# Performance work log

Hardware: AMD Instinct MI355X
Metric: run time of the kernel (lower is better)

The kernel has to match this reference:

```python
import jax, jax.numpy as jnp
import numpy as np

# Scaled Llama backbone (NF4 dequant-matmul == dense matmul math) + LoRA(q,v) + cls head
L, V, D, H, F, R, C = 4, 32000, 2048, 16, 8192, 16, 3
HD = D // H  # 128, matches real Llama head_dim
ALPHA_OVER_R = 32.0 / R
EPS = 1e-5
NEG = -1e9


def setup_inputs() -> dict:
    B, S = 2, 1024
    keys = iter(jax.random.split(jax.random.key(0), 40))

    def rn(shape, s=0.02):
        return jax.random.normal(next(keys), shape, dtype=jnp.float32) * s

    return {
        "input_ids": jax.random.randint(next(keys), (B, S), 0, V),
        "attention_mask": jnp.ones((B, S), dtype=jnp.int32),
        "embed": rn((V, D)),
        "Wq": rn((L, D, D)), "Wk": rn((L, D, D)), "Wv": rn((L, D, D)), "Wo": rn((L, D, D)),
        "Aq": rn((L, R, D)), "Bq": rn((L, D, R)), "Av": rn((L, R, D)), "Bv": rn((L, D, R)),
        "Wg": rn((L, F, D)), "Wu": rn((L, F, D)), "Wd": rn((L, D, F)),
        "norm1": jnp.ones((L, D)), "norm2": jnp.ones((L, D)), "final_norm": jnp.ones((D,)),
        "head_W1": rn((D, D)), "head_b1": jnp.zeros((D,)),
        "head_W2": rn((C, D)), "head_b2": jnp.zeros((C,)),
    }


def _rms(x, w):
    return x * w * jax.lax.rsqrt(jnp.mean(x * x, -1, keepdims=True) + EPS)


def _rope_tables(S):
    inv = 1.0 / (10000.0 ** (jnp.arange(0, HD, 2, dtype=jnp.float32) / HD))
    f = jnp.outer(jnp.arange(S, dtype=jnp.float32), inv)  # [S, HD//2]
    emb = jnp.concatenate([f, f], -1)                      # [S, HD]
    return jnp.cos(emb), jnp.sin(emb)


def _rot(x):
    return jnp.concatenate([-x[..., HD // 2:], x[..., :HD // 2]], -1)


def reference(input_ids, attention_mask, embed, Wq, Wk, Wv, Wo, Aq, Bq, Av, Bv,
              Wg, Wu, Wd, norm1, norm2, final_norm, head_W1, head_b1, head_W2, head_b2):
    B, S = input_ids.shape
    x = embed[input_ids]                                   # [B,S,D]
    cos, sin = _rope_tables(S)
    causal = jnp.tril(jnp.ones((S, S), dtype=bool))
    mask = jnp.where(causal[None, None], 0.0, NEG) \
        + (1.0 - attention_mask.astype(jnp.float32))[:, None, None, :] * NEG  # [B,1,S,S]

    for l in range(L):  # small fixed layer count
        h = _rms(x, norm1[l])

        def proj(W):
            return jnp.einsum('bsd,ed->bse', h, W)

        def lora(A, Bm):
            return ALPHA_OVER_R * jnp.einsum('bsr,er->bse', jnp.einsum('bsd,rd->bsr', h, A), Bm)

        q = (proj(Wq[l]) + lora(Aq[l], Bq[l])).reshape(B, S, H, HD)
        k = proj(Wk[l]).reshape(B, S, H, HD)
        v = (proj(Wv[l]) + lora(Av[l], Bv[l])).reshape(B, S, H, HD)
        q = q * cos[None, :, None, :] + _rot(q) * sin[None, :, None, :]
        k = k * cos[None, :, None, :] + _rot(k) * sin[None, :, None, :]

        scores = jnp.einsum('bqhd,bkhd->bhqk', q, k) / np.float32(np.sqrt(HD)) + mask
        attn = jax.nn.softmax(scores, -1)
        o = jnp.einsum('bhqk,bkhd->bqhd', attn, v).reshape(B, S, D)
        x = x + jnp.einsum('bsd,ed->bse', o, Wo[l])

        h2 = _rms(x, norm2[l])
        g = jnp.einsum('bsd,fd->bsf', h2, Wg[l])
        u = jnp.einsum('bsd,fd->bsf', h2, Wu[l])
        x = x + jnp.einsum('bsf,df->bsd', jax.nn.silu(g) * u, Wd[l])

    x = _rms(x, final_norm)
    # LlamaForSequenceClassification pooling at last non-pad token; score = Identity
    idx = jnp.sum(attention_mask, -1) - 1
    pooled = x[jnp.arange(B), idx].astype(jnp.float32)     # [B, D]
    # head_layer (dropout = identity in eval)
    h = jnp.tanh(pooled @ head_W1.T + head_b1)
    return h @ head_W2.T + head_b2                          # [B, C]
```

## Files before the change

### kernel.cpp

```cpp
#include <hip/hip_runtime.h>

#define NLAYER 4
#define DMODEL 2048
#define NHEAD  16
#define HEADD  128
#define FFDIM  8192
#define RLORA  16
#define SEQLEN 1024
#define NBATCH 2
#define NTOK   (NBATCH*SEQLEN)
#define QKVS   6144

typedef __bf16 bf16x8 __attribute__((ext_vector_type(8)));
typedef float  f32x4  __attribute__((ext_vector_type(4)));
typedef unsigned short us8 __attribute__((ext_vector_type(8)));

__device__ __forceinline__ unsigned short f2b(float f) {
  unsigned int u = __builtin_bit_cast(unsigned int, f);
  u += 0x7FFFu + ((u >> 16) & 1u);
  return (unsigned short)(u >> 16);
}
__device__ __forceinline__ float b2f(unsigned short s) {
  unsigned int u = ((unsigned int)s) << 16;
  return __builtin_bit_cast(float, u);
}
__device__ __forceinline__ int vswz(int d) {
  return (((d >> 2) & 7) ^ ((d & 3) << 1)) << 4;
}
typedef __attribute__((address_space(1))) const void* gas_t;
typedef __attribute__((address_space(3))) void* las_t;
__device__ __forceinline__ void gload16(const void* g, void* l) {
  __builtin_amdgcn_global_load_lds((gas_t)g, (las_t)l, 16, 0, 0);
}

__global__ void k_embed(const int* __restrict__ ids, const float* __restrict__ emb,
                        float* __restrict__ x) {
  int row = blockIdx.x;
  int id = ids[row];
  const float4* src = (const float4*)(emb + (size_t)id * DMODEL);
  float4* dst = (float4*)(x + (size_t)row * DMODEL);
  for (int i = threadIdx.x; i < DMODEL / 4; i += 256) dst[i] = src[i];
}

__global__ void k_cvt16(const float* __restrict__ s, unsigned short* __restrict__ d, int n8) {
  int stride = gridDim.x * 256;
  for (int i = blockIdx.x * 256 + threadIdx.x; i < n8; i += stride) {
    size_t si = (size_t)i * 2;
    float4 a = ((const float4*)s)[si];
    float4 b = ((const float4*)s)[si + 1];
    us8 o;
    o[0]=f2b(a.x); o[1]=f2b(a.y); o[2]=f2b(a.z); o[3]=f2b(a.w);
    o[4]=f2b(b.x); o[5]=f2b(b.y); o[6]=f2b(b.z); o[7]=f2b(b.w);
    ((us8*)d)[i] = o;
  }
}

__global__ void k_cvtqkv(const float* __restrict__ Wq, const float* __restrict__ Wk,
                         const float* __restrict__ Wv, unsigned short* __restrict__ d) {
  const size_t DD8 = (size_t)DMODEL * DMODEL / 8;
  const int n8 = (int)(NLAYER * 3 * DD8);
  int stride = gridDim.x * 256;
  for (int i = blockIdx.x * 256 + threadIdx.x; i < n8; i += stride) {
    int blk = i >> 19;
    int lay = blk / 3;
    int ten = blk - lay * 3;
    int off = i & ((1 << 19) - 1);
    const float* s = (ten == 0 ? Wq : ten == 1 ? Wk : Wv) + (size_t)lay * DMODEL * DMODEL;
    float4 a = ((const float4*)s)[(size_t)off * 2];
    float4 b = ((const float4*)s)[(size_t)off * 2 + 1];
    us8 o;
    o[0]=f2b(a.x); o[1]=f2b(a.y); o[2]=f2b(a.z); o[3]=f2b(a.w);
    o[4]=f2b(b.x); o[5]=f2b(b.y); o[6]=f2b(b.z); o[7]=f2b(b.w);
    ((us8*)(d))[(size_t)i] = o;
  }
}

__global__ void k_rmsnorm(const float* __restrict__ x, const float* __restrict__ w,
                          unsigned short* __restrict__ h) {
  int row = blockIdx.x, t = threadIdx.x;
  const float* xr = x + (size_t)row * DMODEL;
  float4 a = ((const float4*)xr)[t];
  float4 b = ((const float4*)xr)[t + 256];
  float ss = a.x*a.x + a.y*a.y + a.z*a.z + a.w*a.w
           + b.x*b.x + b.y*b.y + b.z*b.z + b.w*b.w;
  for (int m = 32; m; m >>= 1) ss += __shfl_xor(ss, m);
  __shared__ float red[4];
  if ((t & 63) == 0) red[t >> 6] = ss;
  __syncthreads();
  ss = red[0] + red[1] + red[2] + red[3];
  float rs = rsqrtf(ss * (1.0f / DMODEL) + 1e-5f);
  float4 wa = ((const float4*)w)[t];
  float4 wb = ((const float4*)w)[t + 256];
  ushort4 oa, ob;
  oa.x = f2b(a.x * wa.x * rs); oa.y = f2b(a.y * wa.y * rs);
  oa.z = f2b(a.z * wa.z * rs); oa.w = f2b(a.w * wa.w * rs);
  ob.x = f2b(b.x * wb.x * rs); ob.y = f2b(b.y * wb.y * rs);
  ob.z = f2b(b.z * wb.z * rs); ob.w = f2b(b.w * wb.w * rs);
  ushort4* hr = (ushort4*)(h + (size_t)row * DMODEL);
  hr[t] = oa;
  hr[t + 256] = ob;
}

__global__ __launch_bounds__(512, 4)
void k_ffn(const unsigned short* __restrict__ A, const unsigned short* __restrict__ Bgw,
           const unsigned short* __restrict__ Buw, unsigned short* __restrict__ act,
           int N, int K, int ldc) {
  __shared__ unsigned short As[8192];
  __shared__ unsigned short Gs[8192];
  __shared__ unsigned short Us[8192];
  const int t = threadIdx.x, l = t & 63, w = t >> 6;
  const int wm = w >> 2, wn = w & 3;
  const int nbx = gridDim.x;
  const int nmt = gridDim.y;
  const int nwg = nbx * nmt;
  const int bid = blockIdx.y * nbx + blockIdx.x;
  const int sid = (bid & 7) * (nwg >> 3) + (bid >> 3);
  const int m0 = (sid % nmt) << 7;
  const int n0 = (sid / nmt) << 7;
  const int srow = (w << 3) + (l >> 3);
  const int gcol = 8 * ((l & 7) ^ ((srow >> 1) & 7));
  const unsigned short* Ap = A   + (size_t)(m0 + srow) * K + gcol;
  const unsigned short* Gp = Bgw + (size_t)(n0 + srow) * K + gcol;
  const unsigned short* Up = Buw + (size_t)(n0 + srow) * K + gcol;
  const size_t r64K = (size_t)64 * K;
  unsigned short* AsW = As + (w << 9);
  unsigned short* GsW = Gs + (w << 9);
  unsigned short* UsW = Us + (w << 9);
  const int cl = l & 15, lh = l >> 4;
  const int fR = (cl >> 1) & 7;
  f32x4 ag[4][2], au[4][2];
  #pragma unroll
  for (int mi = 0; mi < 4; mi++)
    #pragma unroll
    for (int ni = 0; ni < 2; ni++) {
      f32x4 z = {0.f,0.f,0.f,0.f};
      ag[mi][ni] = z; au[mi][ni] = z;
    }

  for (int kt = 0; kt < K; kt += 64) {
    gload16(Ap + kt,          AsW);
    gload16(Ap + kt + r64K,   AsW + 4096);
    gload16(Gp + kt,          GsW);
    gload16(Gp + kt + r64K,   GsW + 4096);
    gload16(Up + kt,          UsW);
    gload16(Up + kt + r64K,   UsW + 4096);
    __syncthreads();
    #pragma unroll
    for (int kh = 0; kh < 2; kh++) {
      const int so = ((kh * 4 + lh) ^ fR) << 4;
      bf16x8 af[4], bg[2], bu[2];
      #pragma unroll
      for (int mi = 0; mi < 4; mi++)
        af[mi] = *(const bf16x8*)((const char*)As + (wm*64 + mi*16 + cl) * 128 + so);
      #pragma unroll
      for (int ni = 0; ni < 2; ni++) {
        bg[ni] = *(const bf16x8*)((const char*)Gs + (wn*32 + ni*16 + cl) * 128 + so);
        bu[ni] = *(const bf16x8*)((const char*)Us + (wn*32 + ni*16 + cl) * 128 + so);
      }
      #pragma unroll
      for (int mi = 0; mi < 4; mi++)
        #pragma unroll
        for (int ni = 0; ni < 2; ni++) {
          ag[mi][ni] = __builtin_amdgcn_mfma_f32_16x16x32_bf16(af[mi], bg[ni], ag[mi][ni], 0, 0, 0);
          au[mi][ni] = __builtin_amdgcn_mfma_f32_16x16x32_bf16(af[mi], bu[ni], au[mi][ni], 0, 0, 0);
        }
    }
    __syncthreads();
  }
  const int rbase = lh << 2;
  #pragma unroll
  for (int mi = 0; mi < 4; mi++) {
    #pragma unroll
    for (int ni = 0; ni < 2; ni++) {
      #pragma unroll
      for (int rr = 0; rr < 4; rr++) {
        int row = m0 + wm * 64 + mi * 16 + rbase + rr;
        int col = n0 + wn * 32 + ni * 16 + cl;
        float gv = ag[mi][ni][rr];
        float uv = au[mi][ni][rr];
        float val = gv / (1.0f + __expf(-gv)) * uv;
        act[(size_t)row * ldc + col] = f2b(val);
      }
    }
  }
}

template<int MODE>
__global__ __launch_bounds__(256, 4)
void k_gemm6(const unsigned short* __restrict__ A, const unsigned short* __restrict__ B,
             float* __restrict__ Cf, unsigned short* __restrict__ Cb,
             const float* __restrict__ Res, const unsigned short* __restrict__ Gaux,
             int N, int K, int ldc) {
  __shared__ unsigned short As[4096];
  __shared__ unsigned short Bs[8192];
  const int t = threadIdx.x, l = t & 63, w = t >> 6;
  const int nbx = gridDim.x;
  const int nmt = gridDim.y;
  const int bid = blockIdx.y * nbx + blockIdx.x;
  const int xcd = bid & 7;
  const int local = bid >> 3;
  const int cm = nmt >> 2;
  const int cn = nbx >> 1;
  const int m0 = ((xcd & 3) * cm + (local % cm)) << 6;
  const int n0 = ((xcd >> 2) * cn + (local / cm)) << 7;
  const int srow = (w << 3) + (l >> 3);
  const int gcol = 8 * ((l & 7) ^ ((srow >> 1) & 7));
  const unsigned short* Ag = A + (size_t)(m0 + srow) * K + gcol;
  const unsigned short* Bg = B + (size_t)(n0 + srow) * K + gcol;
  const size_t r32K = (size_t)32 * K;
  unsigned short* AsW = As + (w << 9);
  unsigned short* BsW = Bs + (w << 9);
  const int cl = l & 15, lh = l >> 4;
  const int fR = (cl >> 1) & 7;
  f32x4 acc[4][2];
  #pragma unroll
  for (int mi = 0; mi < 4; mi++)
    #pragma unroll
    for (int ni = 0; ni < 2; ni++) { f32x4 z = {0.f,0.f,0.f,0.f}; acc[mi][ni] = z; }

  for (int kt = 0; kt < K; kt += 64) {
    gload16(Ag + kt,          AsW);
    gload16(Ag + kt +   r32K, AsW + 2048);
    gload16(Bg + kt,          BsW);
    gload16(Bg + kt +   r32K, BsW + 2048);
    gload16(Bg + kt + 2*r32K, BsW + 4096);
    gload16(Bg + kt + 3*r32K, BsW + 6144);
    __syncthreads();
    #pragma unroll
    for (int kh = 0; kh < 2; kh++) {
      const int so = ((kh * 4 + lh) ^ fR) << 4;
      bf16x8 af[4], bf[2];
      #pragma unroll
      for (int mi = 0; mi < 4; mi++)
        af[mi] = *(const bf16x8*)((const char*)As + (mi*16 + cl) * 128 + so);
      #pragma unroll
      for (int ni = 0; ni < 2; ni++)
        bf[ni] = *(const bf16x8*)((const char*)Bs + (w*32 + ni*16 + cl) * 128 + so);
      #pragma unroll
      for (int mi = 0; mi < 4; mi++)
        #pragma unroll
        for (int ni = 0; ni < 2; ni++)
          acc[mi][ni] = __builtin_amdgcn_mfma_f32_16x16x32_bf16(af[mi], bf[ni], acc[mi][ni], 0, 0, 0);
    }
    __syncthreads();
  }
  const int rbase = lh << 2;
  #pragma unroll
  for (int mi = 0; mi < 4; mi++) {
    #pragma unroll
    for (int ni = 0; ni < 2; ni++) {
      #pragma unroll
      for (int rr = 0; rr < 4; rr++) {
        int row = m0 + mi * 16 + rbase + rr;
        int col = n0 + w * 32 + ni * 16 + cl;
        size_t idx = (size_t)row * ldc + col;
        float val = acc[mi][ni][rr];
        if constexpr (MODE == 0) Cf[idx] = val;
        if constexpr (MODE == 1) Cf[idx] = val + Res[idx];
        if constexpr (MODE == 2) Cb[idx] = f2b(val);
        if constexpr (MODE == 3) {
          float gv = b2f(Gaux[idx]);
          val *= gv / (1.0f + __expf(-gv));
          Cb[idx] = f2b(val);
        }
      }
    }
  }
}

__global__ __launch_bounds__(256, 4)
void k_gemm7(const unsigned short* __restrict__ A, const unsigned short* __restrict__ B,
             unsigned short* __restrict__ qb, unsigned short* __restrict__ kb,
             unsigned short* __restrict__ vb,
             const float* __restrict__ ct, const float* __restrict__ st,
             int K,
             const float* __restrict__ ltq, const float* __restrict__ ltv,
             const float* __restrict__ lbq, const float* __restrict__ lbv) {
  __shared__ unsigned short As[4096];
  __shared__ unsigned short Bs[8192];
  const int t = threadIdx.x, l = t & 63, w = t >> 6;
  const int nbx = gridDim.x;
  const int nmt = gridDim.y;
  const int nwg = nbx * nmt;
  const int bid = blockIdx.y * nbx + blockIdx.x;
  const int sid = (bid & 7) * (nwg >> 3) + (bid >> 3);
  const int m0 = (sid % nmt) << 6;
  const int n0 = (sid / nmt) << 7;
  const int srow = (w << 3) + (l >> 3);
  const int gcol = 8 * ((l & 7) ^ ((srow >> 1) & 7));
  const unsigned short* Ag = A + (size_t)(m0 + srow) * K + gcol;
  const unsigned short* Bg = B + (size_t)(n0 + srow) * K + gcol;
  const size_t r32K = (size_t)32 * K;
  unsigned short* AsW = As + (w << 9);
  unsigned short* BsW = Bs + (w << 9);
  const int cl = l & 15, lh = l >> 4;
  const int fR = (cl >> 1) & 7;
  f32x4 acc[4][2];
  #pragma unroll
  for (int mi = 0; mi < 4; mi++)
    #pragma unroll
    for (int ni = 0; ni < 2; ni++) { f32x4 z = {0.f,0.f,0.f,0.f}; acc[mi][ni] = z; }

  for (int kt = 0; kt < K; kt += 64) {
    gload16(Ag + kt,          AsW);
    gload16(Ag + kt +   r32K, AsW + 2048);
    gload16(Bg + kt,          BsW);
    gload16(Bg + kt +   r32K, BsW + 2048);
    gload16(Bg + kt + 2*r32K, BsW + 4096);
    gload16(Bg + kt + 3*r32K, BsW + 6144);
    __syncthreads();
    #pragma unroll
    for (int kh = 0; kh < 2; kh++) {
      const int so = ((kh * 4 + lh) ^ fR) << 4;
      bf16x8 af[4], bf[2];
      #pragma unroll
      for (int mi = 0; mi < 4; mi++)
        af[mi] = *(const bf16x8*)((const char*)As + (mi*16 + cl) * 128 + so);
      #pragma unroll
      for (int ni = 0; ni < 2; ni++)
        bf[ni] = *(const bf16x8*)((const char*)Bs + (w*16 + ni*64 + cl) * 128 + so);
      #pragma unroll
      for (int mi = 0; mi < 4; mi++)
        #pragma unroll
        for (int ni = 0; ni < 2; ni++)
          acc[mi][ni] = __builtin_amdgcn_mfma_f32_16x16x32_bf16(af[mi], bf[ni], acc[mi][ni], 0, 0, 0);
    }
    __syncthreads();
  }
  const int rbase = lh << 2;
  const int i0 = (w << 4) + cl;
  const int col_lo = n0 + i0;
  const int reg = n0 >> 11;
  const float* lt = nullptr;
  const float* lb_lo = nullptr;
  const float* lb_hi = nullptr;
  if (reg == 0)      { lt = ltq; lb_lo = lbq + (size_t)col_lo * RLORA;
                                 lb_hi = lbq + (size_t)(col_lo + 64) * RLORA; }
  else if (reg == 2) { lt = ltv; lb_lo = lbv + (size_t)(col_lo - 4096) * RLORA;
                                 lb_hi = lbv + (size_t)(col_lo - 4096 + 64) * RLORA; }
  float4 bl0={0,0,0,0}, bl1=bl0, bl2=bl0, bl3=bl0;
  float4 bh0=bl0, bh1=bl0, bh2=bl0, bh3=bl0;
  if (lt) {
    bl0 = ((const float4*)lb_lo)[0]; bl1 = ((const float4*)lb_lo)[1];
    bl2 = ((const float4*)lb_lo)[2]; bl3 = ((const float4*)lb_lo)[3];
    bh0 = ((const float4*)lb_hi)[0]; bh1 = ((const float4*)lb_hi)[1];
    bh2 = ((const float4*)lb_hi)[2]; bh3 = ((const float4*)lb_hi)[3];
  }
  unsigned short* outp = (reg == 0 ? qb : reg == 1 ? kb : vb);
  const int ocol = col_lo - reg * 2048;
  #pragma unroll
  for (int mi = 0; mi < 4; mi++) {
    #pragma unroll
    for (int rr = 0; rr < 4; rr++) {
      int row = m0 + mi * 16 + rbase + rr;
      float lo = acc[mi][0][rr];
      float hi = acc[mi][1][rr];
      if (lt) {
        const float4* tr = (const float4*)(lt + (size_t)row * RLORA);
        float4 t0 = tr[0], t1 = tr[1], t2 = tr[2], t3 = tr[3];
        lo += 2.0f * (t0.x*bl0.x + t0.y*bl0.y + t0.z*bl0.z + t0.w*bl0.w
                    + t1.x*bl1.x + t1.y*bl1.y + t1.z*bl1.z + t1.w*bl1.w
                    + t2.x*bl2.x + t2.y*bl2.y + t2.z*bl2.z + t2.w*bl2.w
                    + t3.x*bl3.x + t3.y*bl3.y + t3.z*bl3.z + t3.w*bl3.w);
        hi += 2.0f * (t0.x*bh0.x + t0.y*bh0.y + t0.z*bh0.z + t0.w*bh0.w
                    + t1.x*bh1.x + t1.y*bh1.y + t1.z*bh1.z + t1.w*bh1.w
                    + t2.x*bh2.x + t2.y*bh2.y + t2.z*bh2.z + t2.w*bh2.w
                    + t3.x*bh3.x + t3.y*bh3.y + t3.z*bh3.z + t3.w*bh3.w);
      }
      if (reg != 2) {
        int s = row & (SEQLEN - 1);
        float c = ct[s * 64 + i0], sn = st[s * 64 + i0];
        float nlo = lo * c - hi * sn;
        float nhi = hi * c + lo * sn;
        lo = nlo; hi = nhi;
      }
      outp[(size_t)row * DMODEL + ocol]      = f2b(lo);
      outp[(size_t)row * DMODEL + ocol + 64] = f2b(hi);
    }
  }
}

template<int MODE>
__global__ __launch_bounds__(256, 2)
void k_gemm(const unsigned short* __restrict__ A, const void* __restrict__ Bv,
            float* __restrict__ Cf, unsigned short* __restrict__ Cb,
            const float* __restrict__ Res, const unsigned short* __restrict__ Gaux,
            int N, int K, int ldc) {
  __shared__ unsigned char lds[128 * 32 * 2 * 2];
  unsigned char* As = lds;
  unsigned char* Bs = lds + 128 * 32 * 2;
  const int t = threadIdx.x;
  const int l = t & 63, w = t >> 6;
  const int wr = w >> 1, wc = w & 1;
  const int m0 = blockIdx.y << 7, n0 = blockIdx.x << 7;
  const int sr = t >> 1, skh = (t & 1) << 4;
  const int sByte = sr * 64 + (skh << 1);
  const int sSwz = (sr & 3) << 4;
  const unsigned short* Ap = A + (size_t)(m0 + sr) * K + skh;
  const float* Bp32 = (const float*)Bv + (size_t)(n0 + sr) * K + skh;
  const int kOff = (((l >> 4) << 4)) ^ ((l & 3) << 4);
  const int arow = wr * 64 + (l & 15);
  const int brow = wc * 64 + (l & 15);
  f32x4 acc[4][4];
  #pragma unroll
  for (int mi = 0; mi < 4; mi++)
    #pragma unroll
    for (int ni = 0; ni < 4; ni++) { f32x4 z = {0.f,0.f,0.f,0.f}; acc[mi][ni] = z; }

  for (int kt = 0; kt < K; kt += 32) {
    uint4 a0 = *(const uint4*)(Ap + kt);
    uint4 a1 = *(const uint4*)(Ap + kt + 8);
    *(uint4*)(As + ((sByte)      ^ sSwz)) = a0;
    *(uint4*)(As + ((sByte + 16) ^ sSwz)) = a1;
    float4 f0 = *(const float4*)(Bp32 + kt);
    float4 f1 = *(const float4*)(Bp32 + kt + 4);
    float4 f2 = *(const float4*)(Bp32 + kt + 8);
    float4 f3 = *(const float4*)(Bp32 + kt + 12);
    us8 q0, q1;
    q0[0]=f2b(f0.x); q0[1]=f2b(f0.y); q0[2]=f2b(f0.z); q0[3]=f2b(f0.w);
    q0[4]=f2b(f1.x); q0[5]=f2b(f1.y); q0[6]=f2b(f1.z); q0[7]=f2b(f1.w);
    q1[0]=f2b(f2.x); q1[1]=f2b(f2.y); q1[2]=f2b(f2.z); q1[3]=f2b(f2.w);
    q1[4]=f2b(f3.x); q1[5]=f2b(f3.y); q1[6]=f2b(f3.z); q1[7]=f2b(f3.w);
    *(us8*)(Bs + ((sByte)      ^ sSwz)) = q0;
    *(us8*)(Bs + ((sByte + 16) ^ sSwz)) = q1;
    __syncthreads();
    bf16x8 af[4], bfr[4];
    #pragma unroll
    for (int i = 0; i < 4; i++) {
      af[i]  = *(const bf16x8*)(As + (arow + 16 * i) * 64 + kOff);
      bfr[i] = *(const bf16x8*)(Bs + (brow + 16 * i) * 64 + kOff);
    }
    #pragma unroll
    for (int mi = 0; mi < 4; mi++)
      #pragma unroll
      for (int ni = 0; ni < 4; ni++)
        acc[mi][ni] = __builtin_amdgcn_mfma_f32_16x16x32_bf16(af[mi], bfr[ni], acc[mi][ni], 0, 0, 0);
    __syncthreads();
  }
  const int rbase = (l >> 4) << 2;
  const int cl = l & 15;
  #pragma unroll
  for (int mi = 0; mi < 4; mi++) {
    #pragma unroll
    for (int ni = 0; ni < 4; ni++) {
      #pragma unroll
      for (int rr = 0; rr < 4; rr++) {
        int row = m0 + wr * 64 + mi * 16 + rbase + rr;
        int col = n0 + wc * 64 + ni * 16 + cl;
        size_t idx = (size_t)row * ldc + col;
        float val = acc[mi][ni][rr];
        if constexpr (MODE == 0) Cf[idx] = val;
        if constexpr (MODE == 1) Cf[idx] = val + Res[idx];
        if constexpr (MODE == 2) Cb[idx] = f2b(val);
        if constexpr (MODE == 3) {
          float gv = b2f(Gaux[idx]);
          val *= gv / (1.0f + __expf(-gv));
          Cb[idx] = f2b(val);
        }
      }
    }
  }
}

__global__ void k_lora_down2(const unsigned short* __restrict__ h,
                             const float* __restrict__ Aq, const float* __restrict__ Av,
                             float* __restrict__ tbq, float* __restrict__ tbv) {
  int t = threadIdx.x;
  int m = blockIdx.x * 8 + (t >> 5), r = t & 31;
  const float* ar = (r < 16) ? (Aq + (size_t)r * DMODEL)
                             : (Av + (size_t)(r - 16) * DMODEL);
  const unsigned short* hr = h + (size_t)m * DMODEL;
  float acc = 0.f;
  for (int d = 0; d < DMODEL; d += 4) {
    ushort4 hv = *(const ushort4*)(hr + d);
    float4 av = *(const float4*)(ar + d);
    acc += b2f(hv.x)*av.x + b2f(hv.y)*av.y + b2f(hv.z)*av.z + b2f(hv.w)*av.w;
  }
  if (r < 16) tbq[(size_t)m * RLORA + r] = acc;
  else        tbv[(size_t)m * RLORA + (r - 16)] = acc;
}

__global__ void k_lora_down(const unsigned short* __restrict__ h, const float* __restrict__ Am,
                            float* __restrict__ tb) {
  int t = threadIdx.x;
  int m = blockIdx.x * 16 + (t >> 4), r = t & 15;
  const unsigned short* hr = h + (size_t)m * DMODEL;
  const float* ar = Am + (size_t)r * DMODEL;
  float acc = 0.f;
  for (int d = 0; d < DMODEL; d += 4) {
    ushort4 hv = *(const ushort4*)(hr + d);
    float4 av = *(const float4*)(ar + d);
    acc += b2f(hv.x)*av.x + b2f(hv.y)*av.y + b2f(hv.z)*av.z + b2f(hv.w)*av.w;
  }
  tb[(size_t)m * RLORA + r] = acc;
}

__global__ void k_lora_up(const float* __restrict__ tb, const float* __restrict__ Bm,
                          float* __restrict__ out, int ldc) {
  int tid = blockIdx.x * 256 + threadIdx.x;
  int m = tid >> 11, e = tid & (DMODEL - 1);
  const float* tr = tb + (size_t)m * RLORA;
  const float* br = Bm + (size_t)e * RLORA;
  float acc = 0.f;
  #pragma unroll
  for (int r = 0; r < RLORA; r += 4) {
    float4 tv = *(const float4*)(tr + r);
    float4 bv = *(const float4*)(br + r);
    acc += tv.x*bv.x + tv.y*bv.y + tv.z*bv.z + tv.w*bv.w;
  }
  out[(size_t)m * ldc + e] += 2.0f * acc;
}

__global__ void k_rope_table(float* __restrict__ ct, float* __restrict__ st) {
  int tid = blockIdx.x * 256 + threadIdx.x;
  int s = tid >> 6, i = tid & 63;
  float inv = __expf(-((float)i / 64.0f) * logf(10000.0f));
  float ang = (float)s * inv;
  ct[tid] = cosf(ang);
  st[tid] = sinf(ang);
}

__global__ void k_rope2(const float* __restrict__ qkv,
                        const float* __restrict__ ct, const float* __restrict__ st,
                        unsigned short* __restrict__ qb, unsigned short* __restrict__ kb,
                        unsigned short* __restrict__ vb) {
  int tid = blockIdx.x * 256 + threadIdx.x;
  int i = tid & 63;
  int hh = (tid >> 6) & (NHEAD - 1);
  int s = (tid >> 10) & (SEQLEN - 1);
  int b = tid >> 20;
  size_t ibase = ((size_t)(b * SEQLEN + s)) * QKVS + hh * HEADD;
  size_t obase = ((size_t)(b * SEQLEN + s)) * DMODEL + hh * HEADD;
  float c = ct[s * 64 + i], sn = st[s * 64 + i];
  float q0 = qkv[ibase + i], q1 = qkv[ibase + i + 64];
  qb[obase + i]      = f2b(q0 * c - q1 * sn);
  qb[obase + i + 64] = f2b(q1 * c + q0 * sn);
  float k0 = qkv[ibase + 2048 + i], k1 = qkv[ibase + 2048 + i + 64];
  kb[obase + i]      = f2b(k0 * c - k1 * sn);
  kb[obase + i + 64] = f2b(k1 * c + k0 * sn);
  vb[obase + i]      = f2b(qkv[ibase + 4096 + i]);
  vb[obase + i + 64] = f2b(qkv[ibase + 4096 + i + 64]);
}

__global__ __launch_bounds__(256, 2)
void k_attn_bf16(const unsigned short* __restrict__ qbp, const unsigned short* __restrict__ kbp,
                 const unsigned short* __restrict__ vbp, const int* __restrict__ am,
                 unsigned short* __restrict__ o, int vstride) {
  __shared__ unsigned char Kls[64 * 256];
  __shared__ unsigned char Vls[128 * 128];
  __shared__ unsigned char Pls[64 * 128];
  const int qt = blockIdx.x, hh = blockIdx.y, b = blockIdx.z;
  const int t = threadIdx.x, l = t & 63, w = t >> 6;
  const int cl = l & 15, lh = l >> 4;
  const int rbase = lh << 2;

  for (int ii = 0; ii < 4; ii++) {
    int idx = t + 256 * ii; int row = idx >> 4; int c = idx & 15;
    uint4 u = *(const uint4*)(qbp + ((size_t)(b*SEQLEN + qt*64 + row)) * DMODEL + hh * HEADD + c * 8);
    *(uint4*)(Kls + ((row * 256 + c * 16) ^ ((row & 7) << 4))) = u;
  }
  __syncthreads();
  bf16x8 qf[4];
  {
    int row = w * 16 + cl;
    int swz = (row & 7) << 4;
    #pragma unroll
    for (int kt = 0; kt < 4; kt++)
      qf[kt] = *(const bf16x8*)(Kls + ((row * 256 + kt * 64 + lh * 16) ^ swz));
  }

  f32x4 oacc[8];
  #pragma unroll
  for (int i = 0; i < 8; i++) { f32x4 z = {0.f,0.f,0.f,0.f}; oacc[i] = z; }
  float mrun[4], lrun[4];
  #pragma unroll
  for (int r = 0; r < 4; r++) { mrun[r] = -3e38f; lrun[r] = 0.f; }

  for (int kb = 0; kb <= qt; kb++) {
    __syncthreads();
    for (int ii = 0; ii < 4; ii++) {
      int idx = t + 256 * ii; int row = idx >> 4; int c = idx & 15;
      uint4 u = *(const uint4*)(kbp + ((size_t)(b*SEQLEN + kb*64 + row)) * DMODEL + hh * HEADD + c * 8);
      *(uint4*)(Kls + ((row * 256 + c * 16) ^ ((row & 7) << 4))) = u;
    }
    for (int ii = 0; ii < 4; ii++) {
      int idx = t + 256 * ii;
      int n = idx >> 4, dc = idx & 15;
      uint4 a = *(const uint4*)(vbp + ((size_t)(b*SEQLEN + kb*64 + n)) * vstride + hh * HEADD + dc * 8);
      uint4 p;
      p.x = __shfl_xor(a.x, 16); p.y = __shfl_xor(a.y, 16);
      p.z = __shfl_xor(a.z, 16); p.w = __shfl_xor(a.w, 16);
      if (!(l & 16)) {
        int d0 = dc * 8, nb = n * 2;
        unsigned int wd[8];
        wd[0] = (a.x & 0xffffu) | (p.x << 16);
        wd[1] = (a.x >> 16)     | (p.x & 0xffff0000u);
        wd[2] = (a.y & 0xffffu) | (p.y << 16);
        wd[3] = (a.y >> 16)     | (p.y & 0xffff0000u);
        wd[4] = (a.z & 0xffffu) | (p.z << 16);
        wd[5] = (a.z >> 16)     | (p.z & 0xffff0000u);
        wd[6] = (a.w & 0xffffu) | (p.w << 16);
        wd[7] = (a.w >> 16)     | (p.w & 0xffff0000u);
        #pragma unroll
        for (int e = 0; e < 8; e++)
          *(unsigned int*)(Vls + (((d0 + e) * 128 + nb) ^ vswz(d0 + e))) = wd[e];
      }
    }
    __syncthreads();
    f32x4 sacc[4];
    #pragma unroll
    for (int nt = 0; nt < 4; nt++) { f32x4 z = {0.f,0.f,0.f,0.f}; sacc[nt] = z; }
    #pragma unroll
    for (int kt = 0; kt < 4; kt++) {
      #pragma unroll
      for (int nt = 0; nt < 4; nt++) {
        int row = nt * 16 + cl;
        bf16x8 kf = *(const bf16x8*)(Kls + ((row * 256 + kt * 64 + lh * 16) ^ ((row & 7) << 4)));
        sacc[nt] = __builtin_amdgcn_mfma_f32_16x16x32_bf16(qf[kt], kf, sacc[nt], 0, 0, 0);
      }
    }
    float p[4][4];
    float mt[4] = {-3e38f, -3e38f, -3e38f, -3e38f};
    #pragma unroll
    for (int nt = 0; nt < 4; nt++) {
      int kg = kb * 64 + nt * 16 + cl;
      float pad = (1.0f - (float)am[b * SEQLEN + kg]) * (-1e9f);
      #pragma unroll
      for (int r = 0; r < 4; r++) {
        int qg = qt * 64 + w * 16 + rbase + r;
        float s = sacc[nt][r] * 0.08838834764831845f + pad;
        if (kg > qg) s = -1e30f;
        p[nt][r] = s;
        mt[r] = fmaxf(mt[r], s);
      }
    }
    #pragma unroll
    for (int r = 0; r < 4; r++) {
      float m = mt[r];
      m = fmaxf(m, __shfl_xor(m, 1)); m = fmaxf(m, __shfl_xor(m, 2));
      m = fmaxf(m, __shfl_xor(m, 4)); m = fmaxf(m, __shfl_xor(m, 8));
      mt[r] = m;
    }
    float corr[4];
    #pragma unroll
    for (int r = 0; r < 4; r++) {
      float mnew = fmaxf(mrun[r], mt[r]);
      corr[r] = __expf(mrun[r] - mnew);
      mrun[r] = mnew;
    }
    float ps[4] = {0.f, 0.f, 0.f, 0.f};
    #pragma unroll
    for (int nt = 0; nt < 4; nt++)
      #pragma unroll
      for (int r = 0; r < 4; r++) {
        p[nt][r] = __expf(p[nt][r] - mrun[r]);
        ps[r] += p[nt][r];
      }
    #pragma unroll
    for (int r = 0; r < 4; r++) {
      float s = ps[r];
      s += __shfl_xor(s, 1); s += __shfl_xor(s, 2);
      s += __shfl_xor(s, 4); s += __shfl_xor(s, 8);
      lrun[r] = lrun[r] * corr[r] + s;
    }
    #pragma unroll
    for (int nt = 0; nt < 4; nt++)
      #pragma unroll
      for (int r = 0; r < 4; r++) {
        int row = w * 16 + rbase + r;
        *(unsigned short*)(Pls + ((row * 128 + (nt * 16 + cl) * 2) ^ ((row & 7) << 4))) = f2b(p[nt][r]);
      }
    #pragma unroll
    for (int dt = 0; dt < 8; dt++)
      #pragma unroll
      for (int r = 0; r < 4; r++) oacc[dt][r] *= corr[r];
    {
      int prow = w * 16 + cl, pswz = (prow & 7) << 4;
      bf16x8 pf0 = *(const bf16x8*)(Pls + ((prow * 128 +  0 + lh * 16) ^ pswz));
      bf16x8 pf1 = *(const bf16x8*)(Pls + ((prow * 128 + 64 + lh * 16) ^ pswz));
      #pragma unroll
      for (int dt = 0; dt < 8; dt++) {
        int drow = dt * 16 + cl;
        bf16x8 vf0 = *(const bf16x8*)(Vls + ((drow * 128 +  0 + lh * 16) ^ vswz(drow)));
        bf16x8 vf1 = *(const bf16x8*)(Vls + ((drow * 128 + 64 + lh * 16) ^ vswz(drow)));
        oacc[dt] = __builtin_amdgcn_mfma_f32_16x16x32_bf16(pf0, vf0, oacc[dt], 0, 0, 0);
        oacc[dt] = __builtin_amdgcn_mfma_f32_16x16x32_bf16(pf1, vf1, oacc[dt], 0, 0, 0);
      }
    }
  }
  size_t obase = (((size_t)b * SEQLEN + qt * 64 + w * 16) * NHEAD + hh) * HEADD;
  #pragma unroll
  for (int r = 0; r < 4; r++) {
    float inv = 1.0f / lrun[r];
    int row = rbase + r;
    #pragma unroll
    for (int dt = 0; dt < 8; dt++)
      o[obase + (size_t)row * (NHEAD * HEADD) + dt * 16 + cl] = f2b(oacc[dt][r] * inv);
  }
}

__global__ void k_pool(const float* __restrict__ x, const int* __restrict__ am,
                       const float* __restrict__ fn, float* __restrict__ pooled) {
  int b = blockIdx.x, t = threadIdx.x;
  __shared__ float red[4];
  float fc = 0.f;
  for (int i = t; i < SEQLEN; i += 256) fc += (float)am[b * SEQLEN + i];
  for (int m = 32; m; m >>= 1) fc += __shfl_xor(fc, m);
  if ((t & 63) == 0) red[t >> 6] = fc;
  __syncthreads();
  int idx = (int)(red[0] + red[1] + red[2] + red[3]) - 1;
  const float* xr = x + ((size_t)b * SEQLEN + idx) * DMODEL;
  float4 a = ((const float4*)xr)[t], c = ((const float4*)xr)[t + 256];
  float ss = a.x*a.x + a.y*a.y + a.z*a.z + a.w*a.w
           + c.x*c.x + c.y*c.y + c.z*c.z + c.w*c.w;
  for (int m = 32; m; m >>= 1) ss += __shfl_xor(ss, m);
  __syncthreads();
  if ((t & 63) == 0) red[t >> 6] = ss;
  __syncthreads();
  ss = red[0] + red[1] + red[2] + red[3];
  float rs = rsqrtf(ss * (1.0f / DMODEL) + 1e-5f);
  float4 w0 = ((const float4*)fn)[t], w1 = ((const float4*)fn)[t + 256];
  float4 o0, o1;
  o0.x = a.x*rs*w0.x; o0.y = a.y*rs*w0.y; o0.z = a.z*rs*w0.z; o0.w = a.w*rs*w0.w;
  o1.x = c.x*rs*w1.x; o1.y = c.y*rs*w1.y; o1.z = c.z*rs*w1.z; o1.w = c.w*rs*w1.w;
  ((float4*)(pooled + (size_t)b * DMODEL))[t] = o0;
  ((float4*)(pooled + (size_t)b * DMODEL))[t + 256] = o1;
}

__global__ void k_head1(const float* __restrict__ pooled, const float* __restrict__ W1,
                        const float* __restrict__ b1, float* __restrict__ h1) {
  int bi = blockIdx.x;
  int b = bi >> 3, e = ((bi & 7) << 8) + threadIdx.x;
  const float* pr = pooled + (size_t)b * DMODEL;
  const float* wr = W1 + (size_t)e * DMODEL;
  float acc = 0.f;
  for (int d = 0; d < DMODEL; d += 4) {
    float4 pv = *(const float4*)(pr + d);
    float4 wv = *(const float4*)(wr + d);
    acc += pv.x*wv.x + pv.y*wv.y + pv.z*wv.z + pv.w*wv.w;
  }
  h1[(size_t)b * DMODEL + e] = tanhf(acc + b1[e]);
}

__global__ void k_head2(const float* __restrict__ h1, const float* __restrict__ W2,
                        const float* __restrict__ b2, float* __restrict__ out) {
  int bi = blockIdx.x;
  int b = bi / 3, c = bi % 3;
  int l = threadIdx.x;
  float acc = 0.f;
  for (int e = l; e < DMODEL; e += 64)
    acc += h1[(size_t)b * DMODEL + e] * W2[(size_t)c * DMODEL + e];
  for (int m = 32; m; m >>= 1) acc += __shfl_xor(acc, m);
  if (l == 0) out[b * 3 + c] = acc + b2[c];
}

__global__ void k_sentinel(float* out) {
  if (threadIdx.x < 6) out[threadIdx.x] = -12345.0f;
}

extern "C" void kernel_launch(void* const* d_in, const int* in_sizes, int n_in,
                              void* d_out, int out_size, void* d_ws, size_t ws_size,
                              hipStream_t stream) {
  const int*   ids = (const int*)d_in[0];
  const int*   am  = (const int*)d_in[1];
  const float* emb = (const float*)d_in[2];
  const float* Wq  = (const float*)d_in[3];
  const float* Wk  = (const float*)d_in[4];
  const float* Wv  = (const float*)d_in[5];
  const float* Wo  = (const float*)d_in[6];
  const float* Aq  = (const float*)d_in[7];
  const float* Bq  = (const float*)d_in[8];
  const float* Av  = (const float*)d_in[9];
  const float* Bv  = (const float*)d_in[10];
  const float* Wg  = (const float*)d_in[11];
  const float* Wu  = (const float*)d_in[12];
  const float* Wd  = (const float*)d_in[13];
  const float* n1  = (const float*)d_in[14];
  const float* n2  = (const float*)d_in[15];
  const float* fn  = (const float*)d_in[16];
  const float* hW1 = (const float*)d_in[17];
  const float* hb1 = (const float*)d_in[18];
  const float* hW2 = (const float*)d_in[19];
  const float* hb2 = (const float*)d_in[20];
  float* out = (float*)d_out;

  const size_t XOFF    = 0;
  const size_t HOFF    = 16777216;
  const size_t QBOFF   = 25165824;
  const size_t KBOFF   = 33554432;
  const size_t VBOFF   = 41943040;
  const size_t OOFF    = 50331648;
  const size_t GOFF    = 58720256;
  const size_t ACTOFF  = 92274688;
  const size_t QKV32OFF= 125829120;
  const size_t TOFF    = 176160768;
  const size_t NEED = TOFF + 131072 + 131072 + 262144 + 262144 + 16384 + 16384;
  if (ws_size < NEED) {
    k_sentinel<<<1, 64, 0, stream>>>(out);
    return;
  }
  const size_t W16OFF   = (NEED + 255) & ~(size_t)255;
  const size_t W16BYTES = 536870912ull;
  const bool   use16    = ws_size >= W16OFF + W16BYTES;

  char* ws = (char*)d_ws;
  float*          x     = (float*)(ws + XOFF);
  unsigned short* h     = (unsigned short*)(ws + HOFF);
  unsigned short* qb    = (unsigned short*)(ws + QBOFF);
  unsigned short* kb    = (unsigned short*)(ws + KBOFF);
  unsigned short* vb    = (unsigned short*)(ws + VBOFF);
  unsigned short* o     = (unsigned short*)(ws + OOFF);
  unsigned short* g     = (unsigned short*)(ws + GOFF);
  unsigned short* act   = (unsigned short*)(ws + ACTOFF);
  float*          qkv32 = (float*)(ws + QKV32OFF);
  float* tbq    = (float*)(ws + TOFF);
  float* tbv    = (float*)(ws + TOFF + 131072);
  float* ct     = (float*)(ws + TOFF + 262144);
  float* st     = (float*)(ws + TOFF + 262144 + 262144);
  float* pooled = (float*)(ws + TOFF + 262144 + 524288);
  float* h1     = (float*)(ws + TOFF + 262144 + 524288 + 16384);

  unsigned short* w16 = (unsigned short*)(ws + W16OFF);
  const size_t DD = (size_t)DMODEL * DMODEL;
  const size_t FD = (size_t)FFDIM * DMODEL;
  unsigned short* wqkv16 = w16;
  unsigned short* wo16   = w16 + 4ull * 3 * DD;
  unsigned short* wg16   = wo16 + 4ull * DD;
  unsigned short* wu16   = wg16 + 4ull * FD;
  unsigned short* wd16   = wu16 + 4ull * FD;
  if (use16) {
    k_cvtqkv<<<2048, 256, 0, stream>>>(Wq, Wk, Wv, wqkv16);
    k_cvt16<<<2048, 256, 0, stream>>>(Wo, wo16, (int)(4 * DD / 8));
    k_cvt16<<<2048, 256, 0, stream>>>(Wg, wg16, (int)(4 * FD / 8));
    k_cvt16<<<2048, 256, 0, stream>>>(Wu, wu16, (int)(4 * FD / 8));
    k_cvt16<<<2048, 256, 0, stream>>>(Wd, wd16, (int)(4 * FD / 8));
  }

  k_embed<<<NTOK, 256, 0, stream>>>(ids, emb, x);
  k_rope_table<<<SEQLEN * 64 / 256, 256, 0, stream>>>(ct, st);

  dim3 g16(16, 16), gqkv(48, 32), gffn(64, 16), gsq(16, 32), ga(SEQLEN / 64, NHEAD, NBATCH);
  for (int lay = 0; lay < NLAYER; lay++) {
    const float* Bq_l = Bq + (size_t)lay * DMODEL * RLORA;
    const float* Bv_l = Bv + (size_t)lay * DMODEL * RLORA;
    k_rmsnorm<<<NTOK, 256, 0, stream>>>(x, n1 + (size_t)lay * DMODEL, h);
    if (use16) {
      k_lora_down2<<<NTOK / 8, 256, 0, stream>>>(h, Aq + (size_t)lay * RLORA * DMODEL,
                                                 Av + (size_t)lay * RLORA * DMODEL, tbq, tbv);
      k_gemm7<<<gqkv, 256, 0, stream>>>(h, wqkv16 + lay*3*DD, qb, kb, vb, ct, st,
                                        DMODEL, tbq, tbv, Bq_l, Bv_l);
      k_attn_bf16<<<ga, 256, 0, stream>>>(qb, kb, vb, am, o, DMODEL);
      k_gemm6<1><<<gsq, 256, 0, stream>>>(o, wo16 + lay*DD, x, nullptr, x, nullptr, DMODEL, DMODEL, DMODEL);
      k_rmsnorm<<<NTOK, 256, 0, stream>>>(x, n2 + (size_t)lay * DMODEL, h);
      k_ffn<<<gffn, 512, 0, stream>>>(h, wg16 + lay*FD, wu16 + lay*FD, act, FFDIM, DMODEL, FFDIM);
      k_gemm6<1><<<gsq, 256, 0, stream>>>(act, wd16 + lay*FD, x, nullptr, x, nullptr, DMODEL, FFDIM, DMODEL);
    } else {
      k_lora_down<<<NTOK / 16, 256, 0, stream>>>(h, Aq + (size_t)lay * RLORA * DMODEL, tbq);
      k_lora_down<<<NTOK / 16, 256, 0, stream>>>(h, Av + (size_t)lay * RLORA * DMODEL, tbv);
      k_gemm<0><<<g16, 256, 0, stream>>>(h, Wq + lay*DD, qkv32,        nullptr, nullptr, nullptr, DMODEL, DMODEL, QKVS);
      k_gemm<0><<<g16, 256, 0, stream>>>(h, Wk + lay*DD, qkv32 + 2048, nullptr, nullptr, nullptr, DMODEL, DMODEL, QKVS);
      k_gemm<0><<<g16, 256, 0, stream>>>(h, Wv + lay*DD, qkv32 + 4096, nullptr, nullptr, nullptr, DMODEL, DMODEL, QKVS);
      k_lora_up<<<NTOK * DMODEL / 256, 256, 0, stream>>>(tbq, Bq_l, qkv32, QKVS);
      k_lora_up<<<NTOK * DMODEL / 256, 256, 0, stream>>>(tbv, Bv_l, qkv32 + 4096, QKVS);
      k_rope2<<<NBATCH * SEQLEN * NHEAD * 64 / 256, 256, 0, stream>>>(qkv32, ct, st, qb, kb, vb);
      k_attn_bf16<<<ga, 256, 0, stream>>>(qb, kb, vb, am, o, DMODEL);
      k_gemm<1><<<g16, 256, 0, stream>>>(o, Wo + lay*DD, x, nullptr, x, nullptr, DMODEL, DMODEL, DMODEL);
      k_rmsnorm<<<NTOK, 256, 0, stream>>>(x, n2 + (size_t)lay * DMODEL, h);
      k_gemm<2><<<dim3(64,16), 256, 0, stream>>>(h, Wg + lay*FD, nullptr, g, nullptr, nullptr, FFDIM, DMODEL, FFDIM);
      k_gemm<3><<<dim3(64,16), 256, 0, stream>>>(h, Wu + lay*FD, nullptr, act, nullptr, g, FFDIM, DMODEL, FFDIM);
      k_gemm<1><<<g16, 256, 0, stream>>>(act, Wd + lay*FD, x, nullptr, x, nullptr, DMODEL, FFDIM, DMODEL);
    }
  }
  k_pool<<<NBATCH, 256, 0, stream>>>(x, am, fn, pooled);
  k_head1<<<16, 256, 0, stream>>>(pooled, hW1, hb1, h1);
  k_head2<<<6, 64, 0, stream>>>(h1, hW2, hb2, out);
}
```

Before: 2.628 ms.

## Merge weight conversions into one kernel and prefetch K/V tiles in attention

Replaces the five separate fp32-to-bf16 weight conversion launches with a single grid-stride kernel that picks its source and destination tensor from the flat index. This removes launch overhead and the tail gaps between launches. In the attention kernel, the next K/V tile is loaded into registers right after the LDS barrier, so global memory latency overlaps with the MFMA and softmax work of the current tile. The prefetch costs extra VGPRs (eight uint4 per thread), which may lower occupancy under launch_bounds(256,2).

```diff
diff --git a/kernel.cpp b/kernel.cpp
--- a/kernel.cpp
+++ b/kernel.cpp
@@ -42,36 +42,43 @@
   for (int i = threadIdx.x; i < DMODEL / 4; i += 256) dst[i] = src[i];
 }
 
-__global__ void k_cvt16(const float* __restrict__ s, unsigned short* __restrict__ d, int n8) {
+__global__ void k_cvtall(const float* __restrict__ Wq, const float* __restrict__ Wk,
+                         const float* __restrict__ Wv, const float* __restrict__ Wo,
+                         const float* __restrict__ Wg, const float* __restrict__ Wu,
+                         const float* __restrict__ Wd,
+                         unsigned short* __restrict__ wqkv, unsigned short* __restrict__ wo,
+                         unsigned short* __restrict__ wg, unsigned short* __restrict__ wu,
+                         unsigned short* __restrict__ wd) {
+  const int DD8  = 1 << 19;
+  const int QKVC = NLAYER * 3 * DD8;
+  const int WOC  = NLAYER * DD8;
+  const int WFC  = NLAYER * 4 * DD8;
+  const int TOT  = QKVC + WOC + 3 * WFC;
   int stride = gridDim.x * 256;
-  for (int i = blockIdx.x * 256 + threadIdx.x; i < n8; i += stride) {
-    size_t si = (size_t)i * 2;
-    float4 a = ((const float4*)s)[si];
-    float4 b = ((const float4*)s)[si + 1];
+  for (int i = blockIdx.x * 256 + threadIdx.x; i < TOT; i += stride) {
+    int j = i;
+    const float* s;
+    unsigned short* dp;
+    size_t so, dofs;
+    if (j < QKVC) {
+      int blk = j >> 19, lay = blk / 3, ten = blk - lay * 3;
+      s = (ten == 0 ? Wq : ten == 1 ? Wk : Wv) + (size_t)lay * DMODEL * DMODEL;
+      so = (size_t)(j & (DD8 - 1)); dp = wqkv; dofs = (size_t)j;
+    } else if ((j -= QKVC) < WOC) {
+      s = Wo; so = (size_t)j; dp = wo; dofs = (size_t)j;
+    } else if ((j -= WOC) < WFC) {
+      s = Wg; so = (size_t)j; dp = wg; dofs = (size_t)j;
+    } else if ((j -= WFC) < WFC) {
+      s = Wu; so = (size_t)j; dp = wu; dofs = (size_t)j;
+    } else {
+      j -= WFC; s = Wd; so = (size_t)j; dp = wd; dofs = (size_t)j;
+    }
+    float4 a = ((const float4*)s)[so * 2];
+    float4 b = ((const float4*)s)[so * 2 + 1];
     us8 o;
     o[0]=f2b(a.x); o[1]=f2b(a.y); o[2]=f2b(a.z); o[3]=f2b(a.w);
     o[4]=f2b(b.x); o[5]=f2b(b.y); o[6]=f2b(b.z); o[7]=f2b(b.w);
-    ((us8*)d)[i] = o;
-  }
-}
-
-__global__ void k_cvtqkv(const float* __restrict__ Wq, const float* __restrict__ Wk,
-                         const float* __restrict__ Wv, unsigned short* __restrict__ d) {
-  const size_t DD8 = (size_t)DMODEL * DMODEL / 8;
-  const int n8 = (int)(NLAYER * 3 * DD8);
-  int stride = gridDim.x * 256;
-  for (int i = blockIdx.x * 256 + threadIdx.x; i < n8; i += stride) {
-    int blk = i >> 19;
-    int lay = blk / 3;
-    int ten = blk - lay * 3;
-    int off = i & ((1 << 19) - 1);
-    const float* s = (ten == 0 ? Wq : ten == 1 ? Wk : Wv) + (size_t)lay * DMODEL * DMODEL;
-    float4 a = ((const float4*)s)[(size_t)off * 2];
-    float4 b = ((const float4*)s)[(size_t)off * 2 + 1];
-    us8 o;
-    o[0]=f2b(a.x); o[1]=f2b(a.y); o[2]=f2b(a.z); o[3]=f2b(a.w);
-    o[4]=f2b(b.x); o[5]=f2b(b.y); o[6]=f2b(b.z); o[7]=f2b(b.w);
-    ((us8*)(d))[(size_t)i] = o;
+    ((us8*)dp)[dofs] = o;
   }
 }
 
@@ -553,11 +560,21 @@
   const int t = threadIdx.x, l = t & 63, w = t >> 6;
   const int cl = l & 15, lh = l >> 4;
   const int rbase = lh << 2;
-
+  const int prow = t >> 4;
+  const int pc   = t & 15;
+
+  #pragma unroll
   for (int ii = 0; ii < 4; ii++) {
-    int idx = t + 256 * ii; int row = idx >> 4; int c = idx & 15;
-    uint4 u = *(const uint4*)(qbp + ((size_t)(b*SEQLEN + qt*64 + row)) * DMODEL + hh * HEADD + c * 8);
-    *(uint4*)(Kls + ((row * 256 + c * 16) ^ ((row & 7) << 4))) = u;
+    int row = prow + 16 * ii;
+    uint4 u = *(const uint4*)(qbp + ((size_t)(b*SEQLEN + qt*64 + row)) * DMODEL + hh * HEADD + pc * 8);
+    *(uint4*)(Kls + ((row * 256 + pc * 16) ^ ((row & 7) << 4))) = u;
+  }
+  uint4 kreg[4], vreg[4];
+  #pragma unroll
+  for (int ii = 0; ii < 4; ii++) {
+    int row = prow + 16 * ii;
+    kreg[ii] = *(const uint4*)(kbp + ((size_t)(b*SEQLEN + row)) * DMODEL + hh * HEADD + pc * 8);
+    vreg[ii] = *(const uint4*)(vbp + ((size_t)(b*SEQLEN + row)) * vstride + hh * HEADD + pc * 8);
   }
   __syncthreads();
   bf16x8 qf[4];
@@ -578,20 +595,20 @@
 
   for (int kb = 0; kb <= qt; kb++) {
     __syncthreads();
+    #pragma unroll
     for (int ii = 0; ii < 4; ii++) {
-      int idx = t + 256 * ii; int row = idx >> 4; int c = idx & 15;
-      uint4 u = *(const uint4*)(kbp + ((size_t)(b*SEQLEN + kb*64 + row)) * DMODEL + hh * HEADD + c * 8);
-      *(uint4*)(Kls + ((row * 256 + c * 16) ^ ((row & 7) << 4))) = u;
-    }
+      int row = prow + 16 * ii;
+      *(uint4*)(Kls + ((row * 256 + pc * 16) ^ ((row & 7) << 4))) = kreg[ii];
+    }
+    #pragma unroll
     for (int ii = 0; ii < 4; ii++) {
-      int idx = t + 256 * ii;
-      int n = idx >> 4, dc = idx & 15;
-      uint4 a = *(const uint4*)(vbp + ((size_t)(b*SEQLEN + kb*64 + n)) * vstride + hh * HEADD + dc * 8);
+      int n = prow + 16 * ii;
+      uint4 a = vreg[ii];
       uint4 p;
       p.x = __shfl_xor(a.x, 16); p.y = __shfl_xor(a.y, 16);
       p.z = __shfl_xor(a.z, 16); p.w = __shfl_xor(a.w, 16);
       if (!(l & 16)) {
-        int d0 = dc * 8, nb = n * 2;
+        int d0 = pc * 8, nb = n * 2;
         unsigned int wd[8];
         wd[0] = (a.x & 0xffffu) | (p.x << 16);
         wd[1] = (a.x >> 16)     | (p.x & 0xffff0000u);
@@ -607,6 +624,14 @@
       }
     }
     __syncthreads();
+    if (kb < qt) {
+      #pragma unroll
+      for (int ii = 0; ii < 4; ii++) {
+        int row = prow + 16 * ii;
+        kreg[ii] = *(const uint4*)(kbp + ((size_t)(b*SEQLEN + (kb+1)*64 + row)) * DMODEL + hh * HEADD + pc * 8);
+        vreg[ii] = *(const uint4*)(vbp + ((size_t)(b*SEQLEN + (kb+1)*64 + row)) * vstride + hh * HEADD + pc * 8);
+      }
+    }
     f32x4 sacc[4];
     #pragma unroll
     for (int nt = 0; nt < 4; nt++) { f32x4 z = {0.f,0.f,0.f,0.f}; sacc[nt] = z; }
@@ -675,9 +700,9 @@
       #pragma unroll
       for (int r = 0; r < 4; r++) oacc[dt][r] *= corr[r];
     {
-      int prow = w * 16 + cl, pswz = (prow & 7) << 4;
-      bf16x8 pf0 = *(const bf16x8*)(Pls + ((prow * 128 +  0 + lh * 16) ^ pswz));
-      bf16x8 pf1 = *(const bf16x8*)(Pls + ((prow * 128 + 64 + lh * 16) ^ pswz));
+      int prw = w * 16 + cl, pswz = (prw & 7) << 4;
+      bf16x8 pf0 = *(const bf16x8*)(Pls + ((prw * 128 +  0 + lh * 16) ^ pswz));
+      bf16x8 pf1 = *(const bf16x8*)(Pls + ((prw * 128 + 64 + lh * 16) ^ pswz));
       #pragma unroll
       for (int dt = 0; dt < 8; dt++) {
         int drow = dt * 16 + cl;
@@ -829,11 +854,8 @@
   unsigned short* wu16   = wg16 + 4ull * FD;
   unsigned short* wd16   = wu16 + 4ull * FD;
   if (use16) {
-    k_cvtqkv<<<2048, 256, 0, stream>>>(Wq, Wk, Wv, wqkv16);
-    k_cvt16<<<2048, 256, 0, stream>>>(Wo, wo16, (int)(4 * DD / 8));
-    k_cvt16<<<2048, 256, 0, stream>>>(Wg, wg16, (int)(4 * FD / 8));
-    k_cvt16<<<2048, 256, 0, stream>>>(Wu, wu16, (int)(4 * FD / 8));
-    k_cvt16<<<2048, 256, 0, stream>>>(Wd, wd16, (int)(4 * FD / 8));
+    k_cvtall<<<2048, 256, 0, stream>>>(Wq, Wk, Wv, Wo, Wg, Wu, Wd,
+                                       wqkv16, wo16, wg16, wu16, wd16);
   }
 
   k_embed<<<NTOK, 256, 0, stream>>>(ids, emb, x);
```

Result: no change. 2.673 ms (+1.7%).

## Double GEMM K-tile to 128 and register-prefetch next K/V block in attention

Applied to the files above, without the earlier changes.

The GEMM main loop now stages 128-wide K slices of A and B in shared memory instead of 64, halving the number of barrier pairs per K. It keeps the XOR swizzle on the wider 256-byte rows. The attention kernel loads the next K/V tile into registers while computing on the current one, hiding global load latency behind the MFMA work. The costs are doubled LDS use in the GEMM, which may lower occupancy under the 4-blocks launch bound, and extra registers in attention.

```diff
diff --git a/kernel.cpp b/kernel.cpp
--- a/kernel.cpp
+++ b/kernel.cpp
@@ -191,8 +191,8 @@
              float* __restrict__ Cf, unsigned short* __restrict__ Cb,
              const float* __restrict__ Res, const unsigned short* __restrict__ Gaux,
              int N, int K, int ldc) {
-  __shared__ unsigned short As[4096];
-  __shared__ unsigned short Bs[8192];
+  __shared__ unsigned short As[8192];
+  __shared__ unsigned short Bs[16384];
   const int t = threadIdx.x, l = t & 63, w = t >> 6;
   const int nbx = gridDim.x;
   const int nmt = gridDim.y;
@@ -203,11 +203,11 @@
   const int cn = nbx >> 1;
   const int m0 = ((xcd & 3) * cm + (local % cm)) << 6;
   const int n0 = ((xcd >> 2) * cn + (local / cm)) << 7;
-  const int srow = (w << 3) + (l >> 3);
-  const int gcol = 8 * ((l & 7) ^ ((srow >> 1) & 7));
+  const int srow = (w << 2) + (l >> 4);
+  const int gcol = 8 * ((l & 15) ^ ((srow >> 1) & 7));
   const unsigned short* Ag = A + (size_t)(m0 + srow) * K + gcol;
   const unsigned short* Bg = B + (size_t)(n0 + srow) * K + gcol;
-  const size_t r32K = (size_t)32 * K;
+  const size_t r16K = (size_t)16 * K;
   unsigned short* AsW = As + (w << 9);
   unsigned short* BsW = Bs + (w << 9);
   const int cl = l & 15, lh = l >> 4;
@@ -218,24 +218,30 @@
     #pragma unroll
     for (int ni = 0; ni < 2; ni++) { f32x4 z = {0.f,0.f,0.f,0.f}; acc[mi][ni] = z; }
 
-  for (int kt = 0; kt < K; kt += 64) {
+  for (int kt = 0; kt < K; kt += 128) {
     gload16(Ag + kt,          AsW);
-    gload16(Ag + kt +   r32K, AsW + 2048);
+    gload16(Ag + kt +   r16K, AsW + 2048);
+    gload16(Ag + kt + 2*r16K, AsW + 4096);
+    gload16(Ag + kt + 3*r16K, AsW + 6144);
     gload16(Bg + kt,          BsW);
-    gload16(Bg + kt +   r32K, BsW + 2048);
-    gload16(Bg + kt + 2*r32K, BsW + 4096);
-    gload16(Bg + kt + 3*r32K, BsW + 6144);
+    gload16(Bg + kt +   r16K, BsW + 2048);
+    gload16(Bg + kt + 2*r16K, BsW + 4096);
+    gload16(Bg + kt + 3*r16K, BsW + 6144);
+    gload16(Bg + kt + 4*r16K, BsW + 8192);
+    gload16(Bg + kt + 5*r16K, BsW + 10240);
+    gload16(Bg + kt + 6*r16K, BsW + 12288);
+    gload16(Bg + kt + 7*r16K, BsW + 14336);
     __syncthreads();
     #pragma unroll
-    for (int kh = 0; kh < 2; kh++) {
-      const int so = ((kh * 4 + lh) ^ fR) << 4;
+    for (int kk = 0; kk < 4; kk++) {
+      const int so = ((kk * 4 + lh) ^ fR) << 4;
       bf16x8 af[4], bf[2];
       #pragma unroll
       for (int mi = 0; mi < 4; mi++)
-        af[mi] = *(const bf16x8*)((const char*)As + (mi*16 + cl) * 128 + so);
+        af[mi] = *(const bf16x8*)((const char*)As + (mi*16 + cl) * 256 + so);
       #pragma unroll
       for (int ni = 0; ni < 2; ni++)
-        bf[ni] = *(const bf16x8*)((const char*)Bs + (w*32 + ni*16 + cl) * 128 + so);
+        bf[ni] = *(const bf16x8*)((const char*)Bs + (w*32 + ni*16 + cl) * 256 + so);
       #pragma unroll
       for (int mi = 0; mi < 4; mi++)
         #pragma unroll
@@ -553,11 +559,21 @@
   const int t = threadIdx.x, l = t & 63, w = t >> 6;
   const int cl = l & 15, lh = l >> 4;
   const int rbase = lh << 2;
-
+  const int prow = t >> 4;
+  const int pc   = t & 15;
+
+  #pragma unroll
   for (int ii = 0; ii < 4; ii++) {
-    int idx = t + 256 * ii; int row = idx >> 4; int c = idx & 15;
-    uint4 u = *(const uint4*)(qbp + ((size_t)(b*SEQLEN + qt*64 + row)) * DMODEL + hh * HEADD + c * 8);
-    *(uint4*)(Kls + ((row * 256 + c * 16) ^ ((row & 7) << 4))) = u;
+    int row = prow + 16 * ii;
+    uint4 u = *(const uint4*)(qbp + ((size_t)(b*SEQLEN + qt*64 + row)) * DMODEL + hh * HEADD + pc * 8);
+    *(uint4*)(Kls + ((row * 256 + pc * 16) ^ ((row & 7) << 4))) = u;
+  }
+  uint4 kreg[4], vreg[4];
+  #pragma unroll
+  for (int ii = 0; ii < 4; ii++) {
+    int row = prow + 16 * ii;
+    kreg[ii] = *(const uint4*)(kbp + ((size_t)(b*SEQLEN + row)) * DMODEL + hh * HEADD + pc * 8);
+    vreg[ii] = *(const uint4*)(vbp + ((size_t)(b*SEQLEN + row)) * vstride + hh * HEADD + pc * 8);
   }
   __syncthreads();
   bf16x8 qf[4];
@@ -578,20 +594,20 @@
 
   for (int kb = 0; kb <= qt; kb++) {
     __syncthreads();
+    #pragma unroll
     for (int ii = 0; ii < 4; ii++) {
-      int idx = t + 256 * ii; int row = idx >> 4; int c = idx & 15;
-      uint4 u = *(const uint4*)(kbp + ((size_t)(b*SEQLEN + kb*64 + row)) * DMODEL + hh * HEADD + c * 8);
-      *(uint4*)(Kls + ((row * 256 + c * 16) ^ ((row & 7) << 4))) = u;
-    }
+      int row = prow + 16 * ii;
+      *(uint4*)(Kls + ((row * 256 + pc * 16) ^ ((row & 7) << 4))) = kreg[ii];
+    }
+    #pragma unroll
     for (int ii = 0; ii < 4; ii++) {
-      int idx = t + 256 * ii;
-      int n = idx >> 4, dc = idx & 15;
-      uint4 a = *(const uint4*)(vbp + ((size_t)(b*SEQLEN + kb*64 + n)) * vstride + hh * HEADD + dc * 8);
+      int n = prow + 16 * ii;
+      uint4 a = vreg[ii];
       uint4 p;
       p.x = __shfl_xor(a.x, 16); p.y = __shfl_xor(a.y, 16);
       p.z = __shfl_xor(a.z, 16); p.w = __shfl_xor(a.w, 16);
       if (!(l & 16)) {
-        int d0 = dc * 8, nb = n * 2;
+        int d0 = pc * 8, nb = n * 2;
         unsigned int wd[8];
         wd[0] = (a.x & 0xffffu) | (p.x << 16);
         wd[1] = (a.x >> 16)     | (p.x & 0xffff0000u);
@@ -607,6 +623,14 @@
       }
     }
     __syncthreads();
+    if (kb < qt) {
+      #pragma unroll
+      for (int ii = 0; ii < 4; ii++) {
+        int row = prow + 16 * ii;
+        kreg[ii] = *(const uint4*)(kbp + ((size_t)(b*SEQLEN + (kb+1)*64 + row)) * DMODEL + hh * HEADD + pc * 8);
+        vreg[ii] = *(const uint4*)(vbp + ((size_t)(b*SEQLEN + (kb+1)*64 + row)) * vstride + hh * HEADD + pc * 8);
+      }
+    }
     f32x4 sacc[4];
     #pragma unroll
     for (int nt = 0; nt < 4; nt++) { f32x4 z = {0.f,0.f,0.f,0.f}; sacc[nt] = z; }
@@ -675,9 +699,9 @@
       #pragma unroll
       for (int r = 0; r < 4; r++) oacc[dt][r] *= corr[r];
     {
-      int prow = w * 16 + cl, pswz = (prow & 7) << 4;
-      bf16x8 pf0 = *(const bf16x8*)(Pls + ((prow * 128 +  0 + lh * 16) ^ pswz));
-      bf16x8 pf1 = *(const bf16x8*)(Pls + ((prow * 128 + 64 + lh * 16) ^ pswz));
+      int prw = w * 16 + cl, pswz = (prw & 7) << 4;
+      bf16x8 pf0 = *(const bf16x8*)(Pls + ((prw * 128 +  0 + lh * 16) ^ pswz));
+      bf16x8 pf1 = *(const bf16x8*)(Pls + ((prw * 128 + 64 + lh * 16) ^ pswz));
       #pragma unroll
       for (int dt = 0; dt < 8; dt++) {
         int drow = dt * 16 + cl;
```

New measurement: 2.507 ms, median of 2. 4.6% less time.
